# Kernel optimization log

Measured on AMD Instinct MI355X. Metric: run time of the kernel, lower is better.

## Reference

```python
import jax, jax.numpy as jnp
import numpy as np


def _conv1x1(x, w, b):
    # x: (B, C, H, W), w: (O, C), b: (O,) -> (B, O, H, W)
    return jnp.einsum('bchw,oc->bohw', x, w) + b[None, :, None, None]


def setup_inputs() -> dict:
    key = jax.random.key(0)
    ks = jax.random.split(key, 9)
    C, Cb = 256, 128
    B, H, W = 4, 64, 64
    s_in = 1.0 / np.sqrt(C)   # kaiming-uniform-ish scale for 1x1 convs
    s_bn = 1.0 / np.sqrt(Cb)
    return {
        'x': jax.random.normal(ks[0], (B, C, H, W), dtype=jnp.float32),
        'theta_w': jax.random.uniform(ks[1], (Cb, C), jnp.float32, -s_in, s_in),
        'theta_b': jax.random.uniform(ks[2], (Cb,), jnp.float32, -s_in, s_in),
        'phi_w': jax.random.uniform(ks[3], (Cb, C), jnp.float32, -s_in, s_in),
        'phi_b': jax.random.uniform(ks[4], (Cb,), jnp.float32, -s_in, s_in),
        'g_w': jax.random.uniform(ks[5], (Cb, C), jnp.float32, -s_in, s_in),
        'g_b': jax.random.uniform(ks[6], (Cb,), jnp.float32, -s_in, s_in),
        'W_w': jax.random.uniform(ks[7], (C, Cb), jnp.float32, -s_bn, s_bn),
        'W_b': jax.random.uniform(ks[8], (C,), jnp.float32, -s_bn, s_bn),
    }


def reference(x, theta_w, theta_b, phi_w, phi_b, g_w, g_b, W_w, W_b):
    B, C, H, Wd = x.shape
    Cb = theta_w.shape[0]
    # NOTE: the original uses raw torch.reshape (row-major), NOT transpose,
    # so (B, Cb, H, W) -> (B, H*W, Cb) scrambles channel/spatial layout.
    # We replicate that exactly with jnp.reshape.
    theta = _conv1x1(x, theta_w, theta_b).reshape(B, -1, Cb)   # (B, N, Cb)
    phi = _conv1x1(x, phi_w, phi_b).reshape(B, Cb, -1)         # (B, Cb, N)
    g = _conv1x1(x, g_w, g_b).reshape(B, -1, Cb)               # (B, N, Cb)
    scores = jnp.einsum('bnc,bcm->bnm', theta, phi)            # (B, N, N)
    attn = jax.nn.softmax(scores, axis=1)                      # softmax over dim=1 (unusual axis)
    y = jnp.einsum('bnm,bmc->bnc', attn, g)                    # (B, N, Cb)
    y = y.reshape(B, -1, H, Wd)                                # raw reshape back to (B, Cb, H, W)
    w = _conv1x1(y, W_w, W_b)                                  # (B, C, H, W)
    return w + x
```

## Files before the change

kernel.cpp:

```cpp
#include <hip/hip_runtime.h>
#include <math.h>

constexpr int CI = 256;
constexpr int CB = 128;
constexpr int HWD = 4096;
constexpr int NBATCH = 4;
constexpr int NN_ = 4096;
constexpr size_t U1 = (size_t)NBATCH * NN_ * CB;
constexpr size_t U_THETA = 0;
constexpr size_t U_PHIT  = U1;
constexpr size_t U_G     = 2 * U1;
constexpr size_t U_GT    = 3 * U1;
constexpr size_t U_Y     = 4 * U1;
constexpr size_t U_XT    = 4 * U1;
constexpr size_t U_WCAT  = 8 * U1;
constexpr size_t U_WW    = 8 * U1 + 98304;
constexpr size_t F_D     = (8 * U1 + 131072) / 2;

typedef short v8s __attribute__((ext_vector_type(8)));
typedef unsigned short u8s __attribute__((ext_vector_type(8)));
typedef float v4f __attribute__((ext_vector_type(4)));
typedef float v16f __attribute__((ext_vector_type(16)));
#define MFMA16(a, b, c) __builtin_amdgcn_mfma_f32_16x16x32_bf16(a, b, c, 0, 0, 0)
#define MFMA32(a, b, c) __builtin_amdgcn_mfma_f32_32x32x16_bf16(a, b, c, 0, 0, 0)

__device__ __forceinline__ unsigned short f2bf(float f) {
    union { float f; unsigned u; } v; v.f = f;
    unsigned r = v.u + 0x7fff + ((v.u >> 16) & 1);
    return (unsigned short)(r >> 16);
}
__device__ __forceinline__ float bf2f(unsigned short s) {
    union { unsigned u; float f; } v; v.u = (unsigned)s << 16;
    return v.f;
}

__global__ __launch_bounds__(256) void k0_xpose(
    const float* __restrict__ x, unsigned short* __restrict__ xT,
    const float* __restrict__ tw, const float* __restrict__ pw,
    const float* __restrict__ gw, const float* __restrict__ Ww,
    unsigned short* __restrict__ wcat, unsigned short* __restrict__ wwB)
{
    __shared__ unsigned short T[64 * 72];
    const int t = threadIdx.x;
    if (blockIdx.y == 4) {
        int wb = blockIdx.x + 64 * blockIdx.z;
        if (t < 128) {
            int e = (wb * 128 + t) * 4;
            const float* src; unsigned short* dst;
            if (e < 32768)       { src = tw + e;           dst = wcat + e; }
            else if (e < 65536)  { src = pw + (e - 32768); dst = wcat + e; }
            else if (e < 98304)  { src = gw + (e - 65536); dst = wcat + e; }
            else                 { src = Ww + (e - 98304); dst = wwB + (e - 98304); }
            float4 f = *(const float4*)src;
            ushort4 u;
            u.x = f2bf(f.x); u.y = f2bf(f.y); u.z = f2bf(f.z); u.w = f2bf(f.w);
            *(ushort4*)dst = u;
        }
        return;
    }
    const int hw0 = blockIdx.x * 64, c0 = blockIdx.y * 64, b = blockIdx.z;
    const float* xb = x + (size_t)b * CI * HWD;
    const int rr = t >> 4, cc = t & 15;
    #pragma unroll
    for (int pass = 0; pass < 4; pass++) {
        float4 f = *(const float4*)&xb[(size_t)(c0 + pass * 16 + rr) * HWD + hw0 + cc * 4];
        T[(cc * 4 + 0) * 72 + pass * 16 + rr] = f2bf(f.x);
        T[(cc * 4 + 1) * 72 + pass * 16 + rr] = f2bf(f.y);
        T[(cc * 4 + 2) * 72 + pass * 16 + rr] = f2bf(f.z);
        T[(cc * 4 + 3) * 72 + pass * 16 + rr] = f2bf(f.w);
    }
    __syncthreads();
    const int row = t >> 2, cs = (t & 3) * 16;
    unsigned short* dst = xT + (size_t)b * NN_ * CI;
    #pragma unroll
    for (int h = 0; h < 2; h++)
        *(u8s*)&dst[(size_t)(hw0 + row) * CI + c0 + cs + h * 8] =
            *(const u8s*)&T[row * 72 + cs + h * 8];
}

__global__ __launch_bounds__(256, 4) void k1_mfma(
    const unsigned short* __restrict__ xT, const unsigned short* __restrict__ wcat,
    const float* __restrict__ tb, const float* __restrict__ pb,
    const float* __restrict__ gb,
    unsigned short* __restrict__ thetaB, unsigned short* __restrict__ phiTB,
    unsigned short* __restrict__ gB)
{
    __shared__ unsigned short LdsX[64 * 268];
    unsigned short* T = LdsX;
    const int t = threadIdx.x;
    const int lane = t & 63, w = t >> 6;
    const int l31 = lane & 31, lh = lane >> 5;
    const int qj = w >> 1, qh = w & 1;
    const int hw0 = blockIdx.x * 64, j0 = blockIdx.y * 64, b = blockIdx.z;
    const int matId = j0 >> 7, jl0 = j0 & 127;
    const float* bvec = (matId == 0) ? tb : (matId == 1) ? pb : gb;
    const unsigned short* xb = xT + (size_t)b * NN_ * CI;

    {
        const int row = t >> 2, seg = t & 3;
        #pragma unroll
        for (int c8 = 0; c8 < 8; c8++)
            *(u8s*)&LdsX[row * 268 + seg * 64 + c8 * 8] =
                *(const u8s*)&xb[(size_t)(hw0 + row) * CI + seg * 64 + c8 * 8];
    }
    __syncthreads();

    v16f s = {};
    #pragma unroll
    for (int kt = 0; kt < 16; kt++) {
        v8s a = *(const v8s*)&wcat[(size_t)(j0 + qj * 32 + l31) * CI + kt * 16 + lh * 8];
        v8s bx = *(const v8s*)&LdsX[(qh * 32 + l31) * 268 + kt * 16 + lh * 8];
        s = MFMA32(a, bx, s);
    }

    if (matId != 1) {
        unsigned short* dst = ((matId == 0) ? thetaB : gB) + (size_t)b * CB * HWD;
        #pragma unroll
        for (int reg = 0; reg < 16; reg++) {
            int row = (reg & 3) + 8 * (reg >> 2) + 4 * lh;
            int cb = jl0 + qj * 32 + row;
            dst[(size_t)cb * HWD + hw0 + qh * 32 + l31] = f2bf(s[reg] + bvec[cb]);
        }
    } else {
        __syncthreads();
        #pragma unroll
        for (int reg = 0; reg < 16; reg++) {
            int row = (reg & 3) + 8 * (reg >> 2) + 4 * lh;
            T[(qh * 32 + l31) * 76 + qj * 32 + row] =
                f2bf(s[reg] + bvec[jl0 + qj * 32 + row]);
        }
        __syncthreads();
        unsigned short* dst = phiTB + (size_t)b * NN_ * CB;
        const int row = t >> 2, cs = (t & 3) * 16;
        #pragma unroll
        for (int h = 0; h < 2; h++)
            *(u8s*)&dst[(size_t)(hw0 + row) * CB + jl0 + cs + h * 8] =
                *(const u8s*)&T[row * 76 + cs + h * 8];
    }
}

__global__ __launch_bounds__(256, 4) void k2_colsum(
    const unsigned short* __restrict__ thetaB,
    const unsigned short* __restrict__ phiTB,
    float* __restrict__ Dout)
{
    __shared__ unsigned short Lth[64 * 140];
    __shared__ float part[4][32];
    const int t = threadIdx.x;
    const int lane = t & 63, w = t >> 6;
    const int l31 = lane & 31, lh = lane >> 5;
    const int qn = w & 1, qm = w >> 1;
    const int rowS = t >> 4, colS = t & 15;
    const int m0 = blockIdx.x * 64, q = blockIdx.y, b = blockIdx.z;
    const unsigned short* th = thetaB + (size_t)b * NN_ * CB;
    const unsigned short* ph = phiTB + (size_t)b * NN_ * CB;

    v8s bphi[8];
    #pragma unroll
    for (int kt = 0; kt < 8; kt++)
        bphi[kt] = *(const v8s*)&ph[(size_t)(m0 + qm * 32 + l31) * CB + kt * 16 + lh * 8];

    const int nBeg = q * 1024, nEnd = nBeg + 1024;
    #pragma unroll
    for (int pass = 0; pass < 4; pass++)
        *(v8s*)&Lth[(pass * 16 + rowS) * 140 + colS * 8] =
            *(const v8s*)&th[(size_t)(nBeg + pass * 16 + rowS) * CB + colS * 8];
    __syncthreads();

    float dsum = 0.f;
    for (int n0 = nBeg; n0 < nEnd; n0 += 64) {
        int nN = (n0 + 64 < nEnd) ? n0 + 64 : nBeg;
        v8s preg[4];
        #pragma unroll
        for (int pass = 0; pass < 4; pass++)
            preg[pass] = *(const v8s*)&th[(size_t)(nN + pass * 16 + rowS) * CB + colS * 8];
        v16f s = {};
        #pragma unroll
        for (int kt = 0; kt < 8; kt++) {
            v8s ath = *(const v8s*)&Lth[(qn * 32 + l31) * 140 + kt * 16 + lh * 8];
            s = MFMA32(ath, bphi[kt], s);
        }
        __syncthreads();
        #pragma unroll
        for (int pass = 0; pass < 4; pass++)
            *(v8s*)&Lth[(pass * 16 + rowS) * 140 + colS * 8] = preg[pass];
        __syncthreads();
        #pragma unroll
        for (int reg = 0; reg < 16; reg++)
            dsum += __expf(s[reg]);
    }
    dsum += __shfl_xor(dsum, 32);
    if (lane < 32) part[w][l31] = dsum;
    __syncthreads();
    if (t < 64) {
        int qmIdx = t >> 5, j = t & 31;
        float v = part[qmIdx * 2 + 0][j] + part[qmIdx * 2 + 1][j];
        Dout[((size_t)q * NBATCH + b) * NN_ + m0 + qmIdx * 32 + j] = v;
    }
}

__global__ __launch_bounds__(256) void k1b_transpose_scale_g(
    const unsigned short* __restrict__ gB, const float* __restrict__ D,
    unsigned short* __restrict__ gTB)
{
    __shared__ unsigned short T[128 * 36];
    const int t = threadIdx.x;
    const int m0 = blockIdx.x * 32;
    const int b  = blockIdx.z;
    const unsigned short* F = gB + (size_t)b * CB * HWD;
    unsigned short* dst = gTB + (size_t)b * CB * HWD;
    const int mrow = t >> 3, cg = t & 7;
    {
        int m = m0 + mrow;
        float d = D[((size_t)0 * NBATCH + b) * NN_ + m]
                + D[((size_t)1 * NBATCH + b) * NN_ + m]
                + D[((size_t)2 * NBATCH + b) * NN_ + m]
                + D[((size_t)3 * NBATCH + b) * NN_ + m];
        float r = 1.0f / d;
        #pragma unroll
        for (int j8 = 0; j8 < 2; j8++) {
            int cbase = cg * 8 + j8 * 64;
            u8s u = *(const u8s*)&F[(size_t)m * CB + cbase];
            #pragma unroll
            for (int e = 0; e < 8; e++)
                T[(cbase + e) * 36 + mrow] = f2bf(bf2f(u[e]) * r);
        }
    }
    __syncthreads();
    const int c = t >> 1, mh = (t & 1) * 16;
    #pragma unroll
    for (int h8 = 0; h8 < 2; h8++)
        *(u8s*)&dst[(size_t)c * HWD + m0 + mh + h8 * 8] =
            *(const u8s*)&T[c * 36 + mh + h8 * 8];
}

__global__ __launch_bounds__(256, 4) void k3_attn(
    const unsigned short* __restrict__ thetaB,
    const unsigned short* __restrict__ phiTB,
    const unsigned short* __restrict__ gTB,
    unsigned short* __restrict__ Y)
{
    __shared__ unsigned short Lphi[64 * 140];
    __shared__ unsigned short Pl[64 * 76];
    const int t = threadIdx.x;
    const int lane = t & 63, w = t >> 6;
    const int l31 = lane & 31, lh = lane >> 5;
    const int qn = w & 1, qm = w >> 1;
    const int rowS = t >> 4, colS = t & 15;
    const int n0 = blockIdx.x * 64, q = blockIdx.y, b = blockIdx.z;
    const unsigned short* th = thetaB + (size_t)b * NN_ * CB;
    const unsigned short* ph = phiTB + (size_t)b * NN_ * CB;
    const unsigned short* gT = gTB + (size_t)b * CB * HWD;

    v8s ath[8];
    #pragma unroll
    for (int kt = 0; kt < 8; kt++)
        ath[kt] = *(const v8s*)&th[(size_t)(n0 + qn * 32 + l31) * CB + kt * 16 + lh * 8];

    const int mBeg = q * 1024, mEnd = mBeg + 1024;
    #pragma unroll
    for (int pass = 0; pass < 4; pass++)
        *(v8s*)&Lphi[(pass * 16 + rowS) * 140 + colS * 8] =
            *(const v8s*)&ph[(size_t)(mBeg + pass * 16 + rowS) * CB + colS * 8];
    __syncthreads();

    v16f yacc[2] = {};
    for (int m0 = mBeg; m0 < mEnd; m0 += 64) {
        int mN = (m0 + 64 < mEnd) ? m0 + 64 : mBeg;
        v8s preg[4];
        #pragma unroll
        for (int pass = 0; pass < 4; pass++)
            preg[pass] = *(const v8s*)&ph[(size_t)(mN + pass * 16 + rowS) * CB + colS * 8];
        v8s gfrag[4];
        #pragma unroll
        for (int ks = 0; ks < 4; ks++)
            gfrag[ks] = *(const v8s*)&gT[(size_t)(w * 32 + l31) * HWD + m0 + ks * 16 + lh * 8];
        v16f s = {};
        #pragma unroll
        for (int kt = 0; kt < 8; kt++) {
            v8s bphi = *(const v8s*)&Lphi[(qm * 32 + l31) * 140 + kt * 16 + lh * 8];
            s = MFMA32(ath[kt], bphi, s);
        }
        __syncthreads();
        #pragma unroll
        for (int reg = 0; reg < 16; reg++) {
            int row = qn * 32 + (reg & 3) + 8 * (reg >> 2) + 4 * lh;
            Pl[row * 76 + qm * 32 + l31] = f2bf(__expf(s[reg]));
        }
        #pragma unroll
        for (int pass = 0; pass < 4; pass++)
            *(v8s*)&Lphi[(pass * 16 + rowS) * 140 + colS * 8] = preg[pass];
        __syncthreads();
        #pragma unroll
        for (int ks = 0; ks < 4; ks++)
            #pragma unroll
            for (int nt = 0; nt < 2; nt++) {
                v8s ap = *(const v8s*)&Pl[(nt * 32 + l31) * 76 + ks * 16 + lh * 8];
                yacc[nt] = MFMA32(ap, gfrag[ks], yacc[nt]);
            }
    }
    unsigned short* yp = Y + ((size_t)q * NBATCH + b) * CB * HWD;
    #pragma unroll
    for (int nt = 0; nt < 2; nt++)
        #pragma unroll
        for (int reg = 0; reg < 16; reg++) {
            int row = (reg & 3) + 8 * (reg >> 2) + 4 * lh;
            yp[(size_t)(n0 + nt * 32 + row) * CB + w * 32 + l31] = f2bf(yacc[nt][reg]);
        }
}

__global__ __launch_bounds__(256, 2) void k4_mfma(
    const float* __restrict__ x, const unsigned short* __restrict__ wwB,
    const float* __restrict__ Wb, const unsigned short* __restrict__ Ybuf,
    float* __restrict__ out)
{
    __shared__ unsigned short Yt[64 * 136];
    const int t = threadIdx.x;
    const int lane = t & 63, w = t >> 6;
    const int ln = lane & 15, quad = lane >> 4;
    const int hw0 = blockIdx.x * 64, o0 = blockIdx.y * 128, b = blockIdx.z;

    const int cb = t >> 1, seg = (t & 1) * 32;
    #pragma unroll
    for (int g8 = 0; g8 < 4; g8++) {
        float sum[8] = {};
        #pragma unroll
        for (int q = 0; q < 4; q++) {
            u8s u = *(const u8s*)&Ybuf[((size_t)q * NBATCH + b) * CB * HWD +
                                       (size_t)cb * HWD + hw0 + seg + g8 * 8];
            #pragma unroll
            for (int j = 0; j < 8; j++) sum[j] += bf2f(u[j]);
        }
        #pragma unroll
        for (int j = 0; j < 8; j++)
            Yt[(seg + g8 * 8 + j) * 136 + cb] = f2bf(sum[j]);
    }
    __syncthreads();

    v8s aw[2][4];
    #pragma unroll
    for (int os = 0; os < 2; os++)
        #pragma unroll
        for (int kt = 0; kt < 4; kt++)
            aw[os][kt] = *(const v8s*)&wwB[(size_t)(o0 + w * 32 + os * 16 + ln) * CB + kt * 32 + quad * 8];

    v4f s[2][4] = {};
    #pragma unroll
    for (int kt = 0; kt < 4; kt++) {
        v8s by[4];
        #pragma unroll
        for (int mt = 0; mt < 4; mt++)
            by[mt] = *(const v8s*)&Yt[(mt * 16 + ln) * 136 + kt * 32 + quad * 8];
        #pragma unroll
        for (int os = 0; os < 2; os++)
            #pragma unroll
            for (int mt = 0; mt < 4; mt++)
                s[os][mt] = MFMA16(aw[os][kt], by[mt], s[os][mt]);
    }
    #pragma unroll
    for (int os = 0; os < 2; os++)
        #pragma unroll
        for (int mt = 0; mt < 4; mt++)
            #pragma unroll
            for (int r = 0; r < 4; r++) {
                int o = o0 + w * 32 + os * 16 + quad * 4 + r;
                size_t idx = (size_t)b * CI * HWD + (size_t)o * HWD + hw0 + mt * 16 + ln;
                out[idx] = s[os][mt][r] + Wb[o] + x[idx];
            }
}

extern "C" void kernel_launch(void* const* d_in, const int* in_sizes, int n_in,
                              void* d_out, int out_size, void* d_ws, size_t ws_size,
                              hipStream_t stream)
{
    const float* x  = (const float*)d_in[0];
    const float* tw = (const float*)d_in[1];
    const float* tb = (const float*)d_in[2];
    const float* pw = (const float*)d_in[3];
    const float* pb = (const float*)d_in[4];
    const float* gw = (const float*)d_in[5];
    const float* gb = (const float*)d_in[6];
    const float* Ww = (const float*)d_in[7];
    const float* Wb = (const float*)d_in[8];
    unsigned short* wsu = (unsigned short*)d_ws;
    float* wsf = (float*)d_ws;
    unsigned short* thetaB = wsu + U_THETA;
    unsigned short* phiTB  = wsu + U_PHIT;
    unsigned short* gB     = wsu + U_G;
    unsigned short* gTB    = wsu + U_GT;
    unsigned short* Ybuf   = wsu + U_Y;
    unsigned short* xTB    = wsu + U_XT;
    unsigned short* wcatB  = wsu + U_WCAT;
    unsigned short* wwB    = wsu + U_WW;
    float* Dbuf = wsf + F_D;
    float* out = (float*)d_out;
    dim3 blk(256, 1, 1);
    hipLaunchKernelGGL(k0_xpose, dim3(64, 5, NBATCH), blk, 0, stream,
                       x, xTB, tw, pw, gw, Ww, wcatB, wwB);
    hipLaunchKernelGGL(k1_mfma, dim3(64, 6, NBATCH), blk, 0, stream,
                       xTB, wcatB, tb, pb, gb, thetaB, phiTB, gB);
    hipLaunchKernelGGL(k2_colsum, dim3(64, 4, NBATCH), blk, 0, stream,
                       thetaB, phiTB, Dbuf);
    hipLaunchKernelGGL(k1b_transpose_scale_g, dim3(128, 1, NBATCH), blk, 0, stream,
                       gB, Dbuf, gTB);
    hipLaunchKernelGGL(k3_attn, dim3(64, 4, NBATCH), blk, 0, stream,
                       thetaB, phiTB, gTB, Ybuf);
    hipLaunchKernelGGL(k4_mfma, dim3(64, 2, NBATCH), blk, 0, stream,
                       x, wwB, Wb, Ybuf, out);
}
```

Baseline: 195.0 us.

## Fuse softmax column-sum with g transpose-scale into one kernel

Merges the column-sum kernel and the g transpose/scale kernel. Each block now computes the full denominator for 32 columns over all rows, with no split across rows, and immediately scales and transposes g for those columns. This removes a kernel launch and the global round trip of partial denominators. In exchange it launches half as many blocks with larger LDS use and a longer serial loop, which reduces parallelism.

New measurement: 233.2 us. +19.6%, slower.

```diff
diff --git a/kernel.cpp b/kernel.cpp
--- a/kernel.cpp
+++ b/kernel.cpp
@@ -15,7 +15,6 @@
 constexpr size_t U_XT    = 4 * U1;
 constexpr size_t U_WCAT  = 8 * U1;
 constexpr size_t U_WW    = 8 * U1 + 98304;
-constexpr size_t F_D     = (8 * U1 + 131072) / 2;
 
 typedef short v8s __attribute__((ext_vector_type(8)));
 typedef unsigned short u8s __attribute__((ext_vector_type(8)));
@@ -139,51 +138,51 @@
     }
 }
 
-__global__ __launch_bounds__(256, 4) void k2_colsum(
+__global__ __launch_bounds__(256, 2) void k2_colsum_g(
     const unsigned short* __restrict__ thetaB,
     const unsigned short* __restrict__ phiTB,
-    float* __restrict__ Dout)
-{
-    __shared__ unsigned short Lth[64 * 140];
+    const unsigned short* __restrict__ gB,
+    unsigned short* __restrict__ gTB)
+{
+    __shared__ unsigned short Lth[128 * 140];
     __shared__ float part[4][32];
+    __shared__ float Dinv[32];
     const int t = threadIdx.x;
     const int lane = t & 63, w = t >> 6;
     const int l31 = lane & 31, lh = lane >> 5;
-    const int qn = w & 1, qm = w >> 1;
-    const int rowS = t >> 4, colS = t & 15;
-    const int m0 = blockIdx.x * 64, q = blockIdx.y, b = blockIdx.z;
+    const int sRow = t >> 1, sOff = (t & 1) * 64;
+    const int m0 = blockIdx.x * 32, b = blockIdx.z;
     const unsigned short* th = thetaB + (size_t)b * NN_ * CB;
     const unsigned short* ph = phiTB + (size_t)b * NN_ * CB;
 
     v8s bphi[8];
     #pragma unroll
     for (int kt = 0; kt < 8; kt++)
-        bphi[kt] = *(const v8s*)&ph[(size_t)(m0 + qm * 32 + l31) * CB + kt * 16 + lh * 8];
-
-    const int nBeg = q * 1024, nEnd = nBeg + 1024;
-    #pragma unroll
-    for (int pass = 0; pass < 4; pass++)
-        *(v8s*)&Lth[(pass * 16 + rowS) * 140 + colS * 8] =
-            *(const v8s*)&th[(size_t)(nBeg + pass * 16 + rowS) * CB + colS * 8];
+        bphi[kt] = *(const v8s*)&ph[(size_t)(m0 + l31) * CB + kt * 16 + lh * 8];
+
+    #pragma unroll
+    for (int c8 = 0; c8 < 8; c8++)
+        *(u8s*)&Lth[sRow * 140 + sOff + c8 * 8] =
+            *(const u8s*)&th[(size_t)sRow * CB + sOff + c8 * 8];
     __syncthreads();
 
     float dsum = 0.f;
-    for (int n0 = nBeg; n0 < nEnd; n0 += 64) {
-        int nN = (n0 + 64 < nEnd) ? n0 + 64 : nBeg;
-        v8s preg[4];
-        #pragma unroll
-        for (int pass = 0; pass < 4; pass++)
-            preg[pass] = *(const v8s*)&th[(size_t)(nN + pass * 16 + rowS) * CB + colS * 8];
+    for (int it = 0; it < 32; ++it) {
+        const int nN = ((it + 1) & 31) * 128;
+        v8s preg[8];
+        #pragma unroll
+        for (int c8 = 0; c8 < 8; c8++)
+            preg[c8] = *(const v8s*)&th[(size_t)(nN + sRow) * CB + sOff + c8 * 8];
         v16f s = {};
         #pragma unroll
         for (int kt = 0; kt < 8; kt++) {
-            v8s ath = *(const v8s*)&Lth[(qn * 32 + l31) * 140 + kt * 16 + lh * 8];
+            v8s ath = *(const v8s*)&Lth[(w * 32 + l31) * 140 + kt * 16 + lh * 8];
             s = MFMA32(ath, bphi[kt], s);
         }
         __syncthreads();
         #pragma unroll
-        for (int pass = 0; pass < 4; pass++)
-            *(v8s*)&Lth[(pass * 16 + rowS) * 140 + colS * 8] = preg[pass];
+        for (int c8 = 0; c8 < 8; c8++)
+            *(v8s*)&Lth[sRow * 140 + sOff + c8 * 8] = preg[c8];
         __syncthreads();
         #pragma unroll
         for (int reg = 0; reg < 16; reg++)
@@ -192,46 +191,35 @@
     dsum += __shfl_xor(dsum, 32);
     if (lane < 32) part[w][l31] = dsum;
     __syncthreads();
-    if (t < 64) {
-        int qmIdx = t >> 5, j = t & 31;
-        float v = part[qmIdx * 2 + 0][j] + part[qmIdx * 2 + 1][j];
-        Dout[((size_t)q * NBATCH + b) * NN_ + m0 + qmIdx * 32 + j] = v;
-    }
-}
-
-__global__ __launch_bounds__(256) void k1b_transpose_scale_g(
-    const unsigned short* __restrict__ gB, const float* __restrict__ D,
-    unsigned short* __restrict__ gTB)
-{
-    __shared__ unsigned short T[128 * 36];
-    const int t = threadIdx.x;
-    const int m0 = blockIdx.x * 32;
-    const int b  = blockIdx.z;
+    if (t < 32) {
+        float tot = part[0][t] + part[1][t] + part[2][t] + part[3][t];
+        Dinv[t] = 1.0f / tot;
+    }
+    __syncthreads();
+
     const unsigned short* F = gB + (size_t)b * CB * HWD;
     unsigned short* dst = gTB + (size_t)b * CB * HWD;
-    const int mrow = t >> 3, cg = t & 7;
+    unsigned short* T = Lth;
     {
-        int m = m0 + mrow;
-        float d = D[((size_t)0 * NBATCH + b) * NN_ + m]
-                + D[((size_t)1 * NBATCH + b) * NN_ + m]
-                + D[((size_t)2 * NBATCH + b) * NN_ + m]
-                + D[((size_t)3 * NBATCH + b) * NN_ + m];
-        float r = 1.0f / d;
+        const int mrow = t >> 3, cg = t & 7;
+        float r = Dinv[mrow];
         #pragma unroll
         for (int j8 = 0; j8 < 2; j8++) {
             int cbase = cg * 8 + j8 * 64;
-            u8s u = *(const u8s*)&F[(size_t)m * CB + cbase];
+            u8s u = *(const u8s*)&F[(size_t)(m0 + mrow) * CB + cbase];
             #pragma unroll
             for (int e = 0; e < 8; e++)
                 T[(cbase + e) * 36 + mrow] = f2bf(bf2f(u[e]) * r);
         }
     }
     __syncthreads();
-    const int c = t >> 1, mh = (t & 1) * 16;
-    #pragma unroll
-    for (int h8 = 0; h8 < 2; h8++)
-        *(u8s*)&dst[(size_t)c * HWD + m0 + mh + h8 * 8] =
-            *(const u8s*)&T[c * 36 + mh + h8 * 8];
+    {
+        const int c = t >> 1, mh = (t & 1) * 16;
+        #pragma unroll
+        for (int h8 = 0; h8 < 2; h8++)
+            *(u8s*)&dst[(size_t)c * HWD + m0 + mh + h8 * 8] =
+                *(const u8s*)&T[c * 36 + mh + h8 * 8];
+    }
 }
 
 __global__ __launch_bounds__(256, 4) void k3_attn(
@@ -383,7 +371,6 @@
     const float* Ww = (const float*)d_in[7];
     const float* Wb = (const float*)d_in[8];
     unsigned short* wsu = (unsigned short*)d_ws;
-    float* wsf = (float*)d_ws;
     unsigned short* thetaB = wsu + U_THETA;
     unsigned short* phiTB  = wsu + U_PHIT;
     unsigned short* gB     = wsu + U_G;
@@ -392,17 +379,14 @@
     unsigned short* xTB    = wsu + U_XT;
     unsigned short* wcatB  = wsu + U_WCAT;
     unsigned short* wwB    = wsu + U_WW;
-    float* Dbuf = wsf + F_D;
     float* out = (float*)d_out;
     dim3 blk(256, 1, 1);
     hipLaunchKernelGGL(k0_xpose, dim3(64, 5, NBATCH), blk, 0, stream,
                        x, xTB, tw, pw, gw, Ww, wcatB, wwB);
     hipLaunchKernelGGL(k1_mfma, dim3(64, 6, NBATCH), blk, 0, stream,
                        xTB, wcatB, tb, pb, gb, thetaB, phiTB, gB);
-    hipLaunchKernelGGL(k2_colsum, dim3(64, 4, NBATCH), blk, 0, stream,
-                       thetaB, phiTB, Dbuf);
-    hipLaunchKernelGGL(k1b_transpose_scale_g, dim3(128, 1, NBATCH), blk, 0, stream,
-                       gB, Dbuf, gTB);
+    hipLaunchKernelGGL(k2_colsum_g, dim3(128, 1, NBATCH), blk, 0, stream,
+                       thetaB, phiTB, gB, gTB);
     hipLaunchKernelGGL(k3_attn, dim3(64, 4, NBATCH), blk, 0, stream,
                        thetaB, phiTB, gTB, Ybuf);
     hipLaunchKernelGGL(k4_mfma, dim3(64, 2, NBATCH), blk, 0, stream,
```
